# Kernel tuning notes

Hardware: AMD Instinct MI355X
Metric: run time of the kernel (lower is better)

The kernel has to match this reference:

```python
import jax, jax.numpy as jnp
import numpy as np

DT = 0.042
B, L, N_INP, N_HID = 128, 512, 96, 1024


def setup_inputs() -> dict:
    key = jax.random.key(0)
    k_x, k_x2h, k_h2h, k_b, k_g, k_e = jax.random.split(key, 6)
    x = jax.random.normal(k_x, (B, L, N_INP), dtype=jnp.float32)
    # x2h = rand(n_inp, n_hid) * input_scaling (input_scaling = 1.0)
    x2h = jax.random.uniform(k_x2h, (N_INP, N_HID), dtype=jnp.float32)
    # h2h = 2*(2*rand-1) then spectral-norm scaled to rho=0.99; emulate scale statistics
    h2h = 2.0 * (2.0 * jax.random.uniform(k_h2h, (N_HID, N_HID), dtype=jnp.float32) - 1.0)
    # approximate spectral normalization: scale by rho / ||h2h||_2 (power-iteration-free proxy via norm)
    sv = jnp.linalg.norm(h2h, ord=2)
    h2h = h2h * (0.99 / sv)
    bias = (2.0 * jax.random.uniform(k_b, (N_HID,), dtype=jnp.float32) - 1.0)
    # gamma ~ U[2.7, 4.7], epsilon ~ U[4.7, 6.7] per-unit vectors
    gamma = jax.random.uniform(k_g, (N_HID,), dtype=jnp.float32) * 2.0 + 2.7
    epsilon = jax.random.uniform(k_e, (N_HID,), dtype=jnp.float32) * 2.0 + 4.7
    return {"x": x, "x2h": x2h, "h2h": h2h, "bias": bias, "gamma": gamma, "epsilon": epsilon}


def reference(x, x2h, h2h, bias, gamma, epsilon):
    # Precompute input projection for all timesteps: (B, L, H)
    xw = jnp.einsum('bli,ih->blh', x, x2h) + bias
    hy0 = jnp.zeros((x.shape[0], h2h.shape[0]), dtype=x.dtype)
    hz0 = jnp.zeros_like(hy0)

    def step(carry, xt):  # xt: (B, H)
        hy, hz = carry
        hz = hz + DT * (jnp.tanh(xt + hy @ h2h) - gamma * hy - epsilon * hz)
        hy = hy + DT * hz
        return (hy, hz), hy

    (hy, hz), ys = jax.lax.scan(step, (hy0, hz0), jnp.swapaxes(xw, 0, 1))
    all_states = jnp.swapaxes(ys, 0, 1)  # (B, L, H)
    return all_states
```

## Files before the change

### kernel.cpp

```cpp
#include <hip/hip_runtime.h>
#include <math.h>

typedef short short8 __attribute__((ext_vector_type(8)));
typedef float f32x4 __attribute__((ext_vector_type(4)));
typedef unsigned long long u64;
typedef u64 u64x2 __attribute__((ext_vector_type(2)));

#define DT 0.042f
#define LSEQ 512
#define NI 96
#define NH 1024

static __device__ __forceinline__ unsigned short f2bf(float f) {
  unsigned int u = __builtin_bit_cast(unsigned int, f);
  return (unsigned short)((u + 0x7fffu + ((u >> 16) & 1u)) >> 16);
}
static __device__ __forceinline__ float bf2f(unsigned short h) {
  unsigned int u = ((unsigned int)h) << 16;
  return __builtin_bit_cast(float, u);
}
static __device__ __forceinline__ float fast_tanhf(float a) {
  float ax = __builtin_fabsf(a);
  float e = __expf(2.0f * ax);
  float t = 1.0f - 2.0f / (e + 1.0f);
  return a < 0.0f ? -t : t;
}

template <bool F>
static __device__ __forceinline__ void ld16_issue(u64x2* dst, const u64* p) {
  if constexpr (F) {
    asm volatile("global_load_dwordx4 %0, %1, off sc0" : "=v"(*dst) : "v"(p) : "memory");
  } else {
    u64 a = __hip_atomic_load(p, __ATOMIC_RELAXED, __HIP_MEMORY_SCOPE_AGENT);
    u64 b = __hip_atomic_load(p + 1, __ATOMIC_RELAXED, __HIP_MEMORY_SCOPE_AGENT);
    *dst = (u64x2){a, b};
  }
}
template <bool F>
static __device__ __forceinline__ void ld_fence() {
  if constexpr (F) {
    asm volatile("s_waitcnt vmcnt(0)" ::: "memory");
    __builtin_amdgcn_sched_barrier(0);
  }
}
template <bool F>
static __device__ __forceinline__ void stpub(unsigned int* p, unsigned int v) {
  if constexpr (F)
    asm volatile("global_store_dword %0, %1, off sc0" ::"v"(p), "v"(v) : "memory");
  else
    __hip_atomic_store(p, v, __ATOMIC_RELAXED, __HIP_MEMORY_SCOPE_AGENT);
}
static __device__ __forceinline__ void drain_vm() {
  asm volatile("s_waitcnt vmcnt(0)" ::: "memory");
  __builtin_amdgcn_sched_barrier(0);
}
template <bool B> struct BoolC { static constexpr bool value = B; };

__global__ __launch_bounds__(512, 2) void ron_kernel(
    const float* __restrict__ x, const float* __restrict__ x2h,
    const float* __restrict__ h2h, const float* __restrict__ bias,
    const float* __restrict__ gam_, const float* __restrict__ eps_,
    float* __restrict__ out, unsigned int* __restrict__ flags,
    unsigned int* __restrict__ hy_ex) {
  const int tid = threadIdx.x;
  const int w = tid >> 6;
  const int l = tid & 63;
  const int lc = l & 15;
  const int kg = l >> 4;

  __shared__ f32x4 part[2][8][2][64];
  __shared__ int info_sh;

  unsigned int* base = flags + 8192;
  unsigned int* xcdtab = base;
  unsigned int* ctr = base + 256;
  unsigned int* abortw = base + 257;
  unsigned int* enttab = base + 272;

  if (tid == 0) {
    unsigned int myxcd = __builtin_amdgcn_s_getreg(63508) & 15u;
    __hip_atomic_store(xcdtab + blockIdx.x, 0x100u | myxcd, __ATOMIC_RELAXED,
                       __HIP_MEMORY_SCOPE_AGENT);
    __hip_atomic_fetch_add(ctr, 1u, __ATOMIC_RELAXED, __HIP_MEMORY_SCOPE_AGENT);
  }

  if (blockIdx.x == 0 && tid == 0) {
    int gu = 0;
    while (__hip_atomic_load(ctr, __ATOMIC_RELAXED, __HIP_MEMORY_SCOPE_AGENT) < 256u) {
      if (++gu > (1 << 17)) break;
      __builtin_amdgcn_s_sleep(8);
    }
    bool ok = (gu <= (1 << 17));
    unsigned char xs[256];
    if (ok) {
      for (int i = 0; i < 256; ++i) {
        unsigned int v = __hip_atomic_load(xcdtab + i, __ATOMIC_RELAXED, __HIP_MEMORY_SCOPE_AGENT);
        int g2 = 0;
        while (v == 0 && ++g2 <= 8192) {
          __builtin_amdgcn_s_sleep(2);
          v = __hip_atomic_load(xcdtab + i, __ATOMIC_RELAXED, __HIP_MEMORY_SCOPE_AGENT);
        }
        if (v == 0) { ok = false; break; }
        xs[i] = (unsigned char)(v & 15u);
      }
    }
    unsigned int ent[256];
    if (ok) {
      int gidx = 0, nl = 0;
      unsigned char left[256], tmp[256];
      for (unsigned int xc = 0; xc < 16u && gidx < 8; ++xc) {
        int cnt = 0;
        for (int i = 0; i < 256; ++i)
          if (xs[i] == (unsigned char)xc) tmp[cnt++] = (unsigned char)i;
        int p = 0;
        while (cnt - p >= 32 && gidx < 8) {
          for (int k2 = 0; k2 < 32; ++k2)
            ent[tmp[p + k2]] = 1u | ((unsigned)gidx << 1) | ((unsigned)k2 << 4) | (1u << 9);
          ++gidx; p += 32;
        }
        for (; p < cnt; ++p) left[nl++] = tmp[p];
      }
      int li = 0;
      while (gidx < 8) {
        for (int k2 = 0; k2 < 32 && li < nl; ++k2, ++li)
          ent[left[li]] = 1u | ((unsigned)gidx << 1) | ((unsigned)k2 << 4);
        ++gidx;
      }
    } else {
      for (int i = 0; i < 256; ++i)
        ent[i] = 1u | ((unsigned)(i & 7) << 1) | ((unsigned)(i >> 3) << 4);
    }
    for (int i = 0; i < 256; ++i)
      __hip_atomic_store(enttab + i, ent[i], __ATOMIC_RELAXED, __HIP_MEMORY_SCOPE_AGENT);
  }

  if (tid == 0) {
    unsigned int e = 0;
    int gu = 0;
    for (;;) {
      e = __hip_atomic_load(enttab + blockIdx.x, __ATOMIC_RELAXED, __HIP_MEMORY_SCOPE_AGENT);
      if (e || ++gu > (1 << 17)) break;
      __builtin_amdgcn_s_sleep(16);
    }
    if (!e) e = 1u | ((unsigned)(blockIdx.x & 7) << 1) | ((unsigned)(blockIdx.x >> 3) << 4);
    info_sh = (int)e;
  }
  __syncthreads();
  const unsigned int ent = (unsigned int)info_sh;
  const int g = (ent >> 1) & 7;
  const int jb = (ent >> 4) & 31;
  const bool fastm = ((ent >> 9) & 1) != 0;

  short8 wfh[4][2], wfl[4][2];
#pragma unroll
  for (int j = 0; j < 4; ++j) {
    const int krow = (w * 4 + j) * 32 + kg * 8;
#pragma unroll
    for (int t = 0; t < 2; ++t) {
      const int c = jb * 32 + t * 16 + lc;
#pragma unroll
      for (int jj = 0; jj < 8; ++jj) {
        float v = h2h[(size_t)(krow + jj) * NH + c];
        unsigned short hb = f2bf(v);
        wfh[j][t][jj] = (short)hb;
        wfl[j][t][jj] = (short)f2bf(v - bf2f(hb));
      }
    }
  }
  const int myc = jb * 32 + w * 16 + lc;
  short8 xwh[3], xwl[3];
  float bias_c = 0.f, gam = 0.f, ep = 0.f;
  if (w < 2) {
#pragma unroll
    for (int kt = 0; kt < 3; ++kt)
#pragma unroll
      for (int jj = 0; jj < 8; ++jj) {
        float v = x2h[(size_t)(kt * 32 + kg * 8 + jj) * NH + myc];
        unsigned short hb = f2bf(v);
        xwh[kt][jj] = (short)hb;
        xwl[kt][jj] = (short)f2bf(v - bf2f(hb));
      }
    bias_c = bias[myc];
    gam = gam_[myc];
    ep = eps_[myc];
  }

  float hy[4] = {0.f, 0.f, 0.f, 0.f};
  float hz[4] = {0.f, 0.f, 0.f, 0.f};
  const float* xlane = x + (size_t)(g * 16 + lc) * LSEQ * NI + kg * 8;
  const int aoff = lc * 8 + kg * 2;
  unsigned int* myflag = flags + (size_t)(g * 64 + jb * 2 + w) * 16;
  unsigned int* watch =
      flags + (size_t)(g * 64 + (w * 4 + ((l >> 1) & 3)) * 2 + (l & 1)) * 16;
  const int ktc = myc >> 5, kgc = (myc >> 3) & 3, sh = myc & 7;

  f32x4 xr[6];
  if (w < 2) {
#pragma unroll
    for (int kt = 0; kt < 3; ++kt) {
      xr[2 * kt] = *(const f32x4*)(xlane + kt * 32);
      xr[2 * kt + 1] = *(const f32x4*)(xlane + kt * 32 + 4);
    }
  }

  auto run = [&](auto fc) {
    constexpr bool F = decltype(fc)::value;
    bool noSync = false;
    for (int s = 0; s < LSEQ; ++s) {
      const int wb = s % 3;
      const int rb = wb ? wb - 1 : 2;

      short8 axh[3], axl[3];
      if (w < 2) {
#pragma unroll
        for (int kt = 0; kt < 3; ++kt) {
#pragma unroll
          for (int jj = 0; jj < 4; ++jj) {
            unsigned short hb = f2bf(xr[2 * kt][jj]);
            axh[kt][jj] = (short)hb;
            axl[kt][jj] = (short)f2bf(xr[2 * kt][jj] - bf2f(hb));
            unsigned short hb2 = f2bf(xr[2 * kt + 1][jj]);
            axh[kt][jj + 4] = (short)hb2;
            axl[kt][jj + 4] = (short)f2bf(xr[2 * kt + 1][jj] - bf2f(hb2));
          }
        }
      }

      f32x4 a0a = {0.f, 0.f, 0.f, 0.f}, a0b = {0.f, 0.f, 0.f, 0.f};
      f32x4 a1a = {0.f, 0.f, 0.f, 0.f}, a1b = {0.f, 0.f, 0.f, 0.f};
      f32x4 accx = {0.f, 0.f, 0.f, 0.f};
      u64x2 hq[4], lq[4];

      if (s) {
        if (!noSync) {
          int guard = 0;
          for (;;) {
            unsigned int v = __hip_atomic_load(watch, __ATOMIC_RELAXED, __HIP_MEMORY_SCOPE_AGENT);
            if (!__any((int)v < s)) break;
            if ((++guard & 255) == 0) {
              if (__hip_atomic_load(abortw, __ATOMIC_RELAXED, __HIP_MEMORY_SCOPE_AGENT) != 0u ||
                  guard > (1 << 16)) {
                __hip_atomic_store(abortw, 1u, __ATOMIC_RELAXED, __HIP_MEMORY_SCOPE_AGENT);
                noSync = true;
                break;
              }
            }
            __builtin_amdgcn_s_sleep(1);
          }
        }
        asm volatile("" ::: "memory");

        const u64* srcg = (const u64*)hy_ex + (size_t)(rb * 8 + g) * 8192;
#pragma unroll
        for (int j = 0; j < 4; ++j) {
          const int idx = (w * 4 + j) * 128 + aoff;
          ld16_issue<F>(&hq[j], srcg + idx);
          ld16_issue<F>(&lq[j], srcg + 4096 + idx);
        }
      }

      if (w < 2) {
#pragma unroll
        for (int kt = 0; kt < 3; ++kt) {
          accx = __builtin_amdgcn_mfma_f32_16x16x32_bf16(axh[kt], xwh[kt], accx, 0, 0, 0);
          accx = __builtin_amdgcn_mfma_f32_16x16x32_bf16(axl[kt], xwh[kt], accx, 0, 0, 0);
          accx = __builtin_amdgcn_mfma_f32_16x16x32_bf16(axh[kt], xwl[kt], accx, 0, 0, 0);
        }
      }

      if (s) {
        ld_fence<F>();
#pragma unroll
        for (int j = 0; j < 4; ++j) {
          short8 fh = __builtin_bit_cast(short8, hq[j]);
          short8 fl = __builtin_bit_cast(short8, lq[j]);
          if (j & 1) {
            a0b = __builtin_amdgcn_mfma_f32_16x16x32_bf16(fh, wfh[j][0], a0b, 0, 0, 0);
            a1b = __builtin_amdgcn_mfma_f32_16x16x32_bf16(fh, wfh[j][1], a1b, 0, 0, 0);
            a0b = __builtin_amdgcn_mfma_f32_16x16x32_bf16(fl, wfh[j][0], a0b, 0, 0, 0);
            a1b = __builtin_amdgcn_mfma_f32_16x16x32_bf16(fl, wfh[j][1], a1b, 0, 0, 0);
            a0b = __builtin_amdgcn_mfma_f32_16x16x32_bf16(fh, wfl[j][0], a0b, 0, 0, 0);
            a1b = __builtin_amdgcn_mfma_f32_16x16x32_bf16(fh, wfl[j][1], a1b, 0, 0, 0);
          } else {
            a0a = __builtin_amdgcn_mfma_f32_16x16x32_bf16(fh, wfh[j][0], a0a, 0, 0, 0);
            a1a = __builtin_amdgcn_mfma_f32_16x16x32_bf16(fh, wfh[j][1], a1a, 0, 0, 0);
            a0a = __builtin_amdgcn_mfma_f32_16x16x32_bf16(fl, wfh[j][0], a0a, 0, 0, 0);
            a1a = __builtin_amdgcn_mfma_f32_16x16x32_bf16(fl, wfh[j][1], a1a, 0, 0, 0);
            a0a = __builtin_amdgcn_mfma_f32_16x16x32_bf16(fh, wfl[j][0], a0a, 0, 0, 0);
            a1a = __builtin_amdgcn_mfma_f32_16x16x32_bf16(fh, wfl[j][1], a1a, 0, 0, 0);
          }
        }
      }

      part[s & 1][w][0][l] = a0a + a0b;
      part[s & 1][w][1][l] = a1a + a1b;
      __syncthreads();

      if (w < 2) {
        f32x4 r = accx;
#pragma unroll
        for (int ww = 0; ww < 8; ++ww) r += part[s & 1][ww][w][l];

        unsigned int* dstg = hy_ex + (size_t)(wb * 8 + g) * 16384;
#pragma unroll
        for (int i = 0; i < 4; ++i) {
          float a = r[i] + bias_c;
          float th = fast_tanhf(a);
          hz[i] += DT * (th - gam * hy[i] - ep * hz[i]);
          hy[i] += DT * hz[i];
          const int rr = kg * 4 + i;
          unsigned short hb = f2bf(hy[i]);
          unsigned short lb = f2bf(hy[i] - bf2f(hb));
          unsigned int oh = (unsigned int)__shfl_xor((int)hb, 1, 64);
          unsigned int ol = (unsigned int)__shfl_xor((int)lb, 1, 64);
          if (!(lc & 1)) {
            const int u32idx = (ktc * 512 + rr * 32 + kgc * 8 + sh) >> 1;
            stpub<F>(dstg + u32idx, (unsigned int)hb | (oh << 16));
            stpub<F>(dstg + 8192 + u32idx, (unsigned int)lb | (ol << 16));
          }
        }
        drain_vm();
        if (l == 0)
          __hip_atomic_store(myflag, (unsigned int)(s + 1), __ATOMIC_RELAXED,
                             __HIP_MEMORY_SCOPE_AGENT);

#pragma unroll
        for (int i = 0; i < 4; ++i)
          out[((size_t)(g * 16 + kg * 4 + i) * LSEQ + s) * NH + myc] = hy[i];
        const float* xs2 = xlane + (size_t)(s + 1 < LSEQ ? s + 1 : s) * NI;
#pragma unroll
        for (int kt = 0; kt < 3; ++kt) {
          xr[2 * kt] = *(const f32x4*)(xs2 + kt * 32);
          xr[2 * kt + 1] = *(const f32x4*)(xs2 + kt * 32 + 4);
        }
      }
    }
  };

  if (fastm)
    run(BoolC<true>{});
  else
    run(BoolC<false>{});
}

extern "C" void kernel_launch(void* const* d_in, const int* in_sizes, int n_in,
                              void* d_out, int out_size, void* d_ws, size_t ws_size,
                              hipStream_t stream) {
  const float* x = (const float*)d_in[0];
  const float* x2h = (const float*)d_in[1];
  const float* h2h = (const float*)d_in[2];
  const float* bias = (const float*)d_in[3];
  const float* gam = (const float*)d_in[4];
  const float* eps = (const float*)d_in[5];
  float* out = (float*)d_out;

  unsigned int* flags = (unsigned int*)d_ws;
  unsigned int* hy_ex = (unsigned int*)((char*)d_ws + 65536);

  hipMemsetAsync(d_ws, 0, 65536, stream);

  ron_kernel<<<dim3(256), dim3(512), 0, stream>>>(x, x2h, h2h, bias, gam, eps, out, flags, hy_ex);
}
```

Before: 2.114 ms.

## Warp-specialize recurrent kernel: compute waves own full K, helper waves stream x and output

Blocks shrink from 512 to 256 threads. Two compute waves now each hold the full 1024-deep K slice of h2h in registers, which removes the cross-wave LDS reduction and the per-step __syncthreads. A third wave prefetches x into double-buffered LDS and a fourth writes hy to the output, coordinated through volatile shared counters. The hidden-state exchange loads are split into four software-pipelined chunks with partial vmcnt waits. The non-fast path switches from atomics to sc1 loads and stores. The risks are heavy register pressure from 64 short8 weight fragments and spin-wait coupling between waves.

```diff
diff --git a/kernel.cpp b/kernel.cpp
--- a/kernel.cpp
+++ b/kernel.cpp
@@ -27,36 +27,34 @@
 }
 
 template <bool F>
-static __device__ __forceinline__ void ld16_issue(u64x2* dst, const u64* p) {
-  if constexpr (F) {
-    asm volatile("global_load_dwordx4 %0, %1, off sc0" : "=v"(*dst) : "v"(p) : "memory");
-  } else {
-    u64 a = __hip_atomic_load(p, __ATOMIC_RELAXED, __HIP_MEMORY_SCOPE_AGENT);
-    u64 b = __hip_atomic_load(p + 1, __ATOMIC_RELAXED, __HIP_MEMORY_SCOPE_AGENT);
-    *dst = (u64x2){a, b};
-  }
+static __device__ __forceinline__ void ld16(u64x2* d, const void* p) {
+  if constexpr (F)
+    asm volatile("global_load_dwordx4 %0, %1, off sc0" : "=v"(*d) : "v"(p) : "memory");
+  else
+    asm volatile("global_load_dwordx4 %0, %1, off sc1" : "=v"(*d) : "v"(p) : "memory");
 }
 template <bool F>
-static __device__ __forceinline__ void ld_fence() {
-  if constexpr (F) {
-    asm volatile("s_waitcnt vmcnt(0)" ::: "memory");
-    __builtin_amdgcn_sched_barrier(0);
-  }
-}
-template <bool F>
-static __device__ __forceinline__ void stpub(unsigned int* p, unsigned int v) {
+static __device__ __forceinline__ void st4(unsigned int* p, unsigned int v) {
   if constexpr (F)
     asm volatile("global_store_dword %0, %1, off sc0" ::"v"(p), "v"(v) : "memory");
   else
-    __hip_atomic_store(p, v, __ATOMIC_RELAXED, __HIP_MEMORY_SCOPE_AGENT);
-}
-static __device__ __forceinline__ void drain_vm() {
+    asm volatile("global_store_dword %0, %1, off sc1" ::"v"(p), "v"(v) : "memory");
+}
+static __device__ __forceinline__ void vmw16() {
+  asm volatile("s_waitcnt vmcnt(16)" ::: "memory");
+  __builtin_amdgcn_sched_barrier(0);
+}
+static __device__ __forceinline__ void vmw0() {
   asm volatile("s_waitcnt vmcnt(0)" ::: "memory");
   __builtin_amdgcn_sched_barrier(0);
 }
+static __device__ __forceinline__ void lgkm0() {
+  asm volatile("s_waitcnt lgkmcnt(0)" ::: "memory");
+  __builtin_amdgcn_sched_barrier(0);
+}
 template <bool B> struct BoolC { static constexpr bool value = B; };
 
-__global__ __launch_bounds__(512, 2) void ron_kernel(
+__global__ __launch_bounds__(256, 1) void ron_kernel(
     const float* __restrict__ x, const float* __restrict__ x2h,
     const float* __restrict__ h2h, const float* __restrict__ bias,
     const float* __restrict__ gam_, const float* __restrict__ eps_,
@@ -68,8 +66,10 @@
   const int lc = l & 15;
   const int kg = l >> 4;
 
-  __shared__ f32x4 part[2][8][2][64];
   __shared__ int info_sh;
+  __shared__ volatile int xseq, hyseq0, hyseq1, xcons0, xcons1, outsq;
+  __shared__ float xbuf[2][16][NI];
+  __shared__ float hybuf[2][2][16][16];
 
   unsigned int* base = flags + 8192;
   unsigned int* xcdtab = base;
@@ -78,6 +78,7 @@
   unsigned int* enttab = base + 272;
 
   if (tid == 0) {
+    xseq = 0; hyseq0 = 0; hyseq1 = 0; xcons0 = 0; xcons1 = 0; outsq = 0;
     unsigned int myxcd = __builtin_amdgcn_s_getreg(63508) & 15u;
     __hip_atomic_store(xcdtab + blockIdx.x, 0x100u | myxcd, __ATOMIC_RELAXED,
                        __HIP_MEMORY_SCOPE_AGENT);
@@ -151,85 +152,142 @@
   const int jb = (ent >> 4) & 31;
   const bool fastm = ((ent >> 9) & 1) != 0;
 
-  short8 wfh[4][2], wfl[4][2];
-#pragma unroll
-  for (int j = 0; j < 4; ++j) {
-    const int krow = (w * 4 + j) * 32 + kg * 8;
-#pragma unroll
-    for (int t = 0; t < 2; ++t) {
-      const int c = jb * 32 + t * 16 + lc;
-#pragma unroll
-      for (int jj = 0; jj < 8; ++jj) {
-        float v = h2h[(size_t)(krow + jj) * NH + c];
-        unsigned short hb = f2bf(v);
-        wfh[j][t][jj] = (short)hb;
-        wfl[j][t][jj] = (short)f2bf(v - bf2f(hb));
-      }
-    }
-  }
+  if (w == 2) {
+    for (int s = 0; s < LSEQ; ++s) {
+      if (s >= 2) {
+        int gu = 0;
+        while (xcons0 < s - 1 || xcons1 < s - 1) {
+          if (++gu > (1 << 22)) break;
+          __builtin_amdgcn_s_sleep(1);
+        }
+      }
+      f32x4 v[6];
+#pragma unroll
+      for (int k = 0; k < 6; ++k) {
+        const int u = l + 64 * k;
+        const float* p = x + ((size_t)(g * 16 + u / 24) * LSEQ + s) * NI + (u % 24) * 4;
+        v[k] = *(const f32x4*)p;
+      }
+#pragma unroll
+      for (int k = 0; k < 6; ++k) {
+        const int u = l + 64 * k;
+        *(f32x4*)&xbuf[s & 1][u / 24][(u % 24) * 4] = v[k];
+      }
+      lgkm0();
+      if (l == 0) xseq = s + 1;
+    }
+    return;
+  }
+  if (w == 3) {
+    for (int s = 0; s < LSEQ; ++s) {
+      int gu = 0;
+      while (hyseq0 < s + 1 || hyseq1 < s + 1) {
+        if (++gu > (1 << 22)) break;
+        __builtin_amdgcn_s_sleep(1);
+      }
+      const int row = l >> 2, q = l & 3, wv = q >> 1, c0 = (q & 1) * 8;
+      f32x4 a = *(const f32x4*)&hybuf[s & 1][wv][row][c0];
+      f32x4 b = *(const f32x4*)&hybuf[s & 1][wv][row][c0 + 4];
+      lgkm0();
+      if (l == 0) outsq = s + 1;
+      float* po = out + ((size_t)(g * 16 + row) * LSEQ + s) * NH + jb * 32 + q * 8;
+      *(f32x4*)po = a;
+      *(f32x4*)(po + 4) = b;
+    }
+    return;
+  }
+
+  short8 wfh[32], wfl[32];
   const int myc = jb * 32 + w * 16 + lc;
+#pragma unroll
+  for (int j = 0; j < 32; ++j) {
+    const int krow = j * 32 + kg * 8;
+#pragma unroll
+    for (int jj = 0; jj < 8; ++jj) {
+      float v = h2h[(size_t)(krow + jj) * NH + myc];
+      unsigned short hb = f2bf(v);
+      wfh[j][jj] = (short)hb;
+      wfl[j][jj] = (short)f2bf(v - bf2f(hb));
+    }
+  }
   short8 xwh[3], xwl[3];
-  float bias_c = 0.f, gam = 0.f, ep = 0.f;
-  if (w < 2) {
-#pragma unroll
-    for (int kt = 0; kt < 3; ++kt)
-#pragma unroll
-      for (int jj = 0; jj < 8; ++jj) {
-        float v = x2h[(size_t)(kt * 32 + kg * 8 + jj) * NH + myc];
-        unsigned short hb = f2bf(v);
-        xwh[kt][jj] = (short)hb;
-        xwl[kt][jj] = (short)f2bf(v - bf2f(hb));
-      }
-    bias_c = bias[myc];
-    gam = gam_[myc];
-    ep = eps_[myc];
-  }
+#pragma unroll
+  for (int kt = 0; kt < 3; ++kt)
+#pragma unroll
+    for (int jj = 0; jj < 8; ++jj) {
+      float v = x2h[(size_t)(kt * 32 + kg * 8 + jj) * NH + myc];
+      unsigned short hb = f2bf(v);
+      xwh[kt][jj] = (short)hb;
+      xwl[kt][jj] = (short)f2bf(v - bf2f(hb));
+    }
+  const float bias_c = bias[myc];
+  const float gam = gam_[myc];
+  const float ep = eps_[myc];
 
   float hy[4] = {0.f, 0.f, 0.f, 0.f};
   float hz[4] = {0.f, 0.f, 0.f, 0.f};
-  const float* xlane = x + (size_t)(g * 16 + lc) * LSEQ * NI + kg * 8;
-  const int aoff = lc * 8 + kg * 2;
   unsigned int* myflag = flags + (size_t)(g * 64 + jb * 2 + w) * 16;
-  unsigned int* watch =
-      flags + (size_t)(g * 64 + (w * 4 + ((l >> 1) & 3)) * 2 + (l & 1)) * 16;
-  const int ktc = myc >> 5, kgc = (myc >> 3) & 3, sh = myc & 7;
-
-  f32x4 xr[6];
-  if (w < 2) {
-#pragma unroll
-    for (int kt = 0; kt < 3; ++kt) {
-      xr[2 * kt] = *(const f32x4*)(xlane + kt * 32);
-      xr[2 * kt + 1] = *(const f32x4*)(xlane + kt * 32 + 4);
-    }
+  unsigned int* watch = flags + (size_t)(g * 64 + l) * 16;
+
+#define ISSUE(CC, BH, BL)                                                   \
+  {                                                                         \
+    _Pragma("unroll") for (int jj = 0; jj < 8; ++jj) {                      \
+      const int off = lc * 2048 + ((CC)*8 + jj) * 64 + kg * 16;             \
+      ld16<F>(&BH[jj], srcg + off);                                         \
+      ld16<F>(&BL[jj], srcg + 32768 + off);                                 \
+    }                                                                       \
+  }
+#define CRUNCH(CC, BH, BL)                                                  \
+  {                                                                         \
+    _Pragma("unroll") for (int jj = 0; jj < 8; ++jj) {                      \
+      const int kt = (CC)*8 + jj;                                           \
+      short8 fh = __builtin_bit_cast(short8, BH[jj]);                       \
+      short8 fl = __builtin_bit_cast(short8, BL[jj]);                       \
+      acc[(3 * kt) & 3] =                                                   \
+          __builtin_amdgcn_mfma_f32_16x16x32_bf16(fh, wfh[kt], acc[(3 * kt) & 3], 0, 0, 0);      \
+      acc[(3 * kt + 1) & 3] =                                               \
+          __builtin_amdgcn_mfma_f32_16x16x32_bf16(fl, wfh[kt], acc[(3 * kt + 1) & 3], 0, 0, 0);  \
+      acc[(3 * kt + 2) & 3] =                                               \
+          __builtin_amdgcn_mfma_f32_16x16x32_bf16(fh, wfl[kt], acc[(3 * kt + 2) & 3], 0, 0, 0);  \
+    }                                                                       \
   }
 
   auto run = [&](auto fc) {
     constexpr bool F = decltype(fc)::value;
     bool noSync = false;
     for (int s = 0; s < LSEQ; ++s) {
-      const int wb = s % 3;
-      const int rb = wb ? wb - 1 : 2;
-
-      short8 axh[3], axl[3];
-      if (w < 2) {
-#pragma unroll
-        for (int kt = 0; kt < 3; ++kt) {
-#pragma unroll
-          for (int jj = 0; jj < 4; ++jj) {
-            unsigned short hb = f2bf(xr[2 * kt][jj]);
-            axh[kt][jj] = (short)hb;
-            axl[kt][jj] = (short)f2bf(xr[2 * kt][jj] - bf2f(hb));
-            unsigned short hb2 = f2bf(xr[2 * kt + 1][jj]);
-            axh[kt][jj + 4] = (short)hb2;
-            axl[kt][jj + 4] = (short)f2bf(xr[2 * kt + 1][jj] - bf2f(hb2));
-          }
-        }
-      }
-
-      f32x4 a0a = {0.f, 0.f, 0.f, 0.f}, a0b = {0.f, 0.f, 0.f, 0.f};
-      f32x4 a1a = {0.f, 0.f, 0.f, 0.f}, a1b = {0.f, 0.f, 0.f, 0.f};
-      f32x4 accx = {0.f, 0.f, 0.f, 0.f};
-      u64x2 hq[4], lq[4];
+      const int wb = s % 3, rb = wb ? wb - 1 : 2;
+
+      {
+        int gu = 0;
+        while (xseq < s + 1) {
+          if (++gu > (1 << 22)) break;
+          __builtin_amdgcn_s_sleep(1);
+        }
+      }
+      f32x4 acc[4];
+#pragma unroll
+      for (int i = 0; i < 4; ++i) acc[i] = (f32x4){0.f, 0.f, 0.f, 0.f};
+#pragma unroll
+      for (int kt = 0; kt < 3; ++kt) {
+        f32x4 x0 = *(const f32x4*)&xbuf[s & 1][lc][kt * 32 + kg * 8];
+        f32x4 x1 = *(const f32x4*)&xbuf[s & 1][lc][kt * 32 + kg * 8 + 4];
+        short8 axh, axl;
+#pragma unroll
+        for (int jj = 0; jj < 4; ++jj) {
+          unsigned short hb = f2bf(x0[jj]);
+          axh[jj] = (short)hb;
+          axl[jj] = (short)f2bf(x0[jj] - bf2f(hb));
+          unsigned short hb2 = f2bf(x1[jj]);
+          axh[jj + 4] = (short)hb2;
+          axl[jj + 4] = (short)f2bf(x1[jj] - bf2f(hb2));
+        }
+        acc[(3 * kt) & 3] = __builtin_amdgcn_mfma_f32_16x16x32_bf16(axh, xwh[kt], acc[(3 * kt) & 3], 0, 0, 0);
+        acc[(3 * kt + 1) & 3] = __builtin_amdgcn_mfma_f32_16x16x32_bf16(axl, xwh[kt], acc[(3 * kt + 1) & 3], 0, 0, 0);
+        acc[(3 * kt + 2) & 3] = __builtin_amdgcn_mfma_f32_16x16x32_bf16(axh, xwl[kt], acc[(3 * kt + 2) & 3], 0, 0, 0);
+      }
+      lgkm0();
+      if (l == 0) { if (w == 0) xcons0 = s + 1; else xcons1 = s + 1; }
 
       if (s) {
         if (!noSync) {
@@ -250,90 +308,57 @@
         }
         asm volatile("" ::: "memory");
 
-        const u64* srcg = (const u64*)hy_ex + (size_t)(rb * 8 + g) * 8192;
-#pragma unroll
-        for (int j = 0; j < 4; ++j) {
-          const int idx = (w * 4 + j) * 128 + aoff;
-          ld16_issue<F>(&hq[j], srcg + idx);
-          ld16_issue<F>(&lq[j], srcg + 4096 + idx);
-        }
-      }
-
-      if (w < 2) {
-#pragma unroll
-        for (int kt = 0; kt < 3; ++kt) {
-          accx = __builtin_amdgcn_mfma_f32_16x16x32_bf16(axh[kt], xwh[kt], accx, 0, 0, 0);
-          accx = __builtin_amdgcn_mfma_f32_16x16x32_bf16(axl[kt], xwh[kt], accx, 0, 0, 0);
-          accx = __builtin_amdgcn_mfma_f32_16x16x32_bf16(axh[kt], xwl[kt], accx, 0, 0, 0);
-        }
-      }
-
-      if (s) {
-        ld_fence<F>();
-#pragma unroll
-        for (int j = 0; j < 4; ++j) {
-          short8 fh = __builtin_bit_cast(short8, hq[j]);
-          short8 fl = __builtin_bit_cast(short8, lq[j]);
-          if (j & 1) {
-            a0b = __builtin_amdgcn_mfma_f32_16x16x32_bf16(fh, wfh[j][0], a0b, 0, 0, 0);
-            a1b = __builtin_amdgcn_mfma_f32_16x16x32_bf16(fh, wfh[j][1], a1b, 0, 0, 0);
-            a0b = __builtin_amdgcn_mfma_f32_16x16x32_bf16(fl, wfh[j][0], a0b, 0, 0, 0);
-            a1b = __builtin_amdgcn_mfma_f32_16x16x32_bf16(fl, wfh[j][1], a1b, 0, 0, 0);
-            a0b = __builtin_amdgcn_mfma_f32_16x16x32_bf16(fh, wfl[j][0], a0b, 0, 0, 0);
-            a1b = __builtin_amdgcn_mfma_f32_16x16x32_bf16(fh, wfl[j][1], a1b, 0, 0, 0);
-          } else {
-            a0a = __builtin_amdgcn_mfma_f32_16x16x32_bf16(fh, wfh[j][0], a0a, 0, 0, 0);
-            a1a = __builtin_amdgcn_mfma_f32_16x16x32_bf16(fh, wfh[j][1], a1a, 0, 0, 0);
-            a0a = __builtin_amdgcn_mfma_f32_16x16x32_bf16(fl, wfh[j][0], a0a, 0, 0, 0);
-            a1a = __builtin_amdgcn_mfma_f32_16x16x32_bf16(fl, wfh[j][1], a1a, 0, 0, 0);
-            a0a = __builtin_amdgcn_mfma_f32_16x16x32_bf16(fh, wfl[j][0], a0a, 0, 0, 0);
-            a1a = __builtin_amdgcn_mfma_f32_16x16x32_bf16(fh, wfl[j][1], a1a, 0, 0, 0);
-          }
-        }
-      }
-
-      part[s & 1][w][0][l] = a0a + a0b;
-      part[s & 1][w][1][l] = a1a + a1b;
-      __syncthreads();
-
-      if (w < 2) {
-        f32x4 r = accx;
-#pragma unroll
-        for (int ww = 0; ww < 8; ++ww) r += part[s & 1][ww][w][l];
-
-        unsigned int* dstg = hy_ex + (size_t)(wb * 8 + g) * 16384;
-#pragma unroll
-        for (int i = 0; i < 4; ++i) {
-          float a = r[i] + bias_c;
-          float th = fast_tanhf(a);
-          hz[i] += DT * (th - gam * hy[i] - ep * hz[i]);
-          hy[i] += DT * hz[i];
-          const int rr = kg * 4 + i;
-          unsigned short hb = f2bf(hy[i]);
-          unsigned short lb = f2bf(hy[i] - bf2f(hb));
-          unsigned int oh = (unsigned int)__shfl_xor((int)hb, 1, 64);
-          unsigned int ol = (unsigned int)__shfl_xor((int)lb, 1, 64);
-          if (!(lc & 1)) {
-            const int u32idx = (ktc * 512 + rr * 32 + kgc * 8 + sh) >> 1;
-            stpub<F>(dstg + u32idx, (unsigned int)hb | (oh << 16));
-            stpub<F>(dstg + 8192 + u32idx, (unsigned int)lb | (ol << 16));
-          }
-        }
-        drain_vm();
-        if (l == 0)
-          __hip_atomic_store(myflag, (unsigned int)(s + 1), __ATOMIC_RELAXED,
-                             __HIP_MEMORY_SCOPE_AGENT);
-
-#pragma unroll
-        for (int i = 0; i < 4; ++i)
-          out[((size_t)(g * 16 + kg * 4 + i) * LSEQ + s) * NH + myc] = hy[i];
-        const float* xs2 = xlane + (size_t)(s + 1 < LSEQ ? s + 1 : s) * NI;
-#pragma unroll
-        for (int kt = 0; kt < 3; ++kt) {
-          xr[2 * kt] = *(const f32x4*)(xs2 + kt * 32);
-          xr[2 * kt + 1] = *(const f32x4*)(xs2 + kt * 32 + 4);
-        }
-      }
+        const char* srcg = (const char*)hy_ex + (size_t)(rb * 8 + g) * 65536;
+        u64x2 Ah0[8], Al0[8], Ah1[8], Al1[8];
+        ISSUE(0, Ah0, Al0);
+        ISSUE(1, Ah1, Al1);
+        vmw16();
+        CRUNCH(0, Ah0, Al0);
+        ISSUE(2, Ah0, Al0);
+        vmw16();
+        CRUNCH(1, Ah1, Al1);
+        ISSUE(3, Ah1, Al1);
+        vmw16();
+        CRUNCH(2, Ah0, Al0);
+        vmw0();
+        CRUNCH(3, Ah1, Al1);
+      }
+
+      f32x4 r = (acc[0] + acc[1]) + (acc[2] + acc[3]);
+      unsigned int* dstg = hy_ex + (size_t)(wb * 8 + g) * 16384;
+#pragma unroll
+      for (int i = 0; i < 4; ++i) {
+        float a = r[i] + bias_c;
+        float th = fast_tanhf(a);
+        hz[i] += DT * (th - gam * hy[i] - ep * hz[i]);
+        hy[i] += DT * hz[i];
+        const int rr = kg * 4 + i;
+        unsigned short hb = f2bf(hy[i]);
+        unsigned short lb = f2bf(hy[i] - bf2f(hb));
+        unsigned int oh = (unsigned int)__shfl_xor((int)hb, 1, 64);
+        unsigned int ol = (unsigned int)__shfl_xor((int)lb, 1, 64);
+        if (!(lc & 1)) {
+          const int u32i = rr * 512 + (myc >> 1);
+          st4<F>(dstg + u32i, (unsigned int)hb | (oh << 16));
+          st4<F>(dstg + 8192 + u32i, (unsigned int)lb | (ol << 16));
+        }
+      }
+      vmw0();
+      if (l == 0)
+        __hip_atomic_store(myflag, (unsigned int)(s + 1), __ATOMIC_RELAXED,
+                           __HIP_MEMORY_SCOPE_AGENT);
+
+      if (s >= 2) {
+        int gu = 0;
+        while (outsq < s - 1) {
+          if (++gu > (1 << 22)) break;
+          __builtin_amdgcn_s_sleep(1);
+        }
+      }
+#pragma unroll
+      for (int i = 0; i < 4; ++i) hybuf[s & 1][w][kg * 4 + i][lc] = hy[i];
+      lgkm0();
+      if (l == 0) { if (w == 0) hyseq0 = s + 1; else hyseq1 = s + 1; }
     }
   };
 
@@ -341,6 +366,8 @@
     run(BoolC<true>{});
   else
     run(BoolC<false>{});
+#undef ISSUE
+#undef CRUNCH
 }
 
 extern "C" void kernel_launch(void* const* d_in, const int* in_sizes, int n_in,
@@ -359,5 +386,5 @@
 
   hipMemsetAsync(d_ws, 0, 65536, stream);
 
-  ron_kernel<<<dim3(256), dim3(512), 0, stream>>>(x, x2h, h2h, bias, gam, eps, out, flags, hy_ex);
-}
+  ron_kernel<<<dim3(256), dim3(256), 0, stream>>>(x, x2h, h2h, bias, gam, eps, out, flags, hy_ex);
+}
```

Measured after the change: 3.342 ms. +58.1%, slower.
